# Performance work log

Hardware: AMD Instinct MI355X
Metric: run time of the kernel (lower is better)

The kernel has to match this reference:

```python
import jax, jax.numpy as jnp
import numpy as np

B, T, E = 4, 2048, 2048
H, KV = 16, 4
G = H // KV           # GQA group size
D = E // H            # head_dim = 128


def setup_inputs() -> dict:
    key = jax.random.key(0)
    kx, kq, kk, kv, ko = jax.random.split(key, 5)
    s = 1.0 / np.sqrt(E).astype(np.float32)
    x  = jax.random.normal(kx, (B, T, E), jnp.float32)
    Wq = jax.random.normal(kq, (E, H * D), jnp.float32) * s
    Wk = jax.random.normal(kk, (E, KV * D), jnp.float32) * s
    Wv = jax.random.normal(kv, (E, KV * D), jnp.float32) * s
    Wo = jax.random.normal(ko, (H * D, E), jnp.float32) * s
    return {"x": x, "Wq": Wq, "Wk": Wk, "Wv": Wv, "Wo": Wo}


def reference(x, Wq, Wk, Wv, Wo):
    # causal=True (default in the torch module)
    b, t, _ = x.shape
    scale = 1.0 / np.sqrt(D).astype(np.float32)
    # q heads ordered so that reshape (H,)->(KV,G) matches torch repeat_interleave
    q = (x @ Wq).reshape(b, t, KV, G, D)   # (B,T,KV,G,D)
    k = (x @ Wk).reshape(b, t, KV, D)      # (B,T,KV,D)
    v = (x @ Wv).reshape(b, t, KV, D)
    # scores per (kv-head h, group member g): (B,KV,G,T,T)
    scores = jnp.einsum('bqhgd,bkhd->bhgqk', q, k) * scale
    causal_mask = jnp.tril(jnp.ones((t, t), dtype=bool))  # True = keep
    scores = jnp.where(causal_mask, scores, -jnp.inf)
    w = jax.nn.softmax(scores, axis=-1)
    y = jnp.einsum('bhgqk,bkhd->bqhgd', w, v)  # (B,T,KV,G,D)
    y = y.reshape(b, t, H * D)
    return y @ Wo
```

## Files before the change

kernel.cpp:

```cpp
#include <hip/hip_runtime.h>

typedef unsigned short u16;
typedef __attribute__((ext_vector_type(8))) __bf16 bf16x8;
typedef __attribute__((ext_vector_type(4))) float f32x4;

#define BB 4
#define TT 2048
#define EE 2048
#define HH 16
#define KVH 4
#define DD 128

static __device__ __forceinline__ u16 f2bf(float f) {
  unsigned int u = __float_as_uint(f);
  u += 0x7fffu + ((u >> 16) & 1u);
  return (u16)(u >> 16);
}

static __device__ __forceinline__ void gl_lds16(const u16* g, u16* l) {
  __builtin_amdgcn_global_load_lds((__attribute__((address_space(1))) void*)g,
                                   (__attribute__((address_space(3))) void*)l,
                                   16, 0, 0);
}

__global__ __launch_bounds__(256) void cvt_f32_bf16(const float* __restrict__ in,
                                                    u16* __restrict__ out, int n4) {
  int i = blockIdx.x * 256 + threadIdx.x;
  if (i >= n4) return;
  float4 v = ((const float4*)in)[i];
  union { uint2 u2; u16 s[4]; } o;
  o.s[0] = f2bf(v.x); o.s[1] = f2bf(v.y); o.s[2] = f2bf(v.z); o.s[3] = f2bf(v.w);
  ((uint2*)out)[i] = o.u2;
}

__global__ __launch_bounds__(256) void transpose_w(const float* __restrict__ W,
                                                   u16* __restrict__ Wt, int R, int C) {
  __shared__ float tile[32][33];
  int tx = threadIdx.x & 31, ty = threadIdx.x >> 5;
  int r0 = blockIdx.y * 32, c0 = blockIdx.x * 32;
  #pragma unroll
  for (int i = ty; i < 32; i += 8)
    tile[i][tx] = W[(size_t)(r0 + i) * C + (c0 + tx)];
  __syncthreads();
  #pragma unroll
  for (int i = ty; i < 32; i += 8)
    Wt[(size_t)(c0 + i) * R + (r0 + tx)] = f2bf(tile[tx][i]);
}

__global__ __launch_bounds__(256) void transpose_v(const u16* __restrict__ KVb,
                                                   u16* __restrict__ VTg) {
  __shared__ u16 tile[32][36];
  const int tid = threadIdx.x;
  const int t0 = blockIdx.x * 32, d0 = blockIdx.y * 32;
  const int z = blockIdx.z;
  const int vb = z * 128;
  const size_t srcbase = (size_t)(z >> 2) * TT * 1024 + 512 + (z & 3) * 128;
  {
    int i = tid >> 3, c4 = (tid & 7) * 4;
    union { uint2 u; u16 s[4]; } r;
    r.u = *(const uint2*)(KVb + srcbase + (size_t)(t0 + i) * 1024 + d0 + c4);
    tile[i][c4] = r.s[0]; tile[i][c4 + 1] = r.s[1];
    tile[i][c4 + 2] = r.s[2]; tile[i][c4 + 3] = r.s[3];
  }
  __syncthreads();
  {
    int j = tid >> 3, cc = (tid & 7) * 4;
    union { uint2 u; u16 s[4]; } w;
    w.s[0] = tile[cc][j]; w.s[1] = tile[cc + 1][j];
    w.s[2] = tile[cc + 2][j]; w.s[3] = tile[cc + 3][j];
    *(uint2*)(VTg + (size_t)(vb + d0 + j) * TT + t0 + cc) = w.u;
  }
}

template <int MODE>
__global__ __launch_bounds__(512) void gemm256(const u16* __restrict__ A,
                                               const u16* __restrict__ Bt0,
                                               const u16* __restrict__ Bt1,
                                               void* __restrict__ C0,
                                               void* __restrict__ C1,
                                               int M, int N0, int N1, int K, int nbx) {
  __shared__ __align__(16) u16 sh[2][4][8192];
  const int tid = threadIdx.x;
  const int lane = tid & 63, wave = tid >> 6;
  const int quad = lane >> 4, n16 = lane & 15;
  const int mi = wave >> 2, ni = wave & 3;

  const int nwg = gridDim.x;
  int wg = blockIdx.x;
  wg = (wg & 7) * (nwg >> 3) + (wg >> 3);
  const int bx = wg % nbx, by = wg / nbx;
  const size_t rowbase = (size_t)by * 256;
  const int colbase = bx * 256;

  const u16* Bt = Bt0;
  int bcol = colbase;
  if (MODE == 1 && colbase >= N0) { Bt = Bt1; bcol = colbase - N0; }

  const int c0 = tid, c1 = tid + 512;
  const int r0s = c0 >> 3, ci0 = (c0 & 7) ^ (r0s & 7);
  const int r1s = c1 >> 3, ci1 = (c1 & 7) ^ (r1s & 7);
  const u16* Ag0 = A + (rowbase + r0s) * (size_t)K + ci0 * 8;
  const u16* Ag1 = A + (rowbase + r1s) * (size_t)K + ci1 * 8;
  const u16* Bg0 = Bt + ((size_t)bcol + r0s) * K + ci0 * 8;
  const u16* Bg1 = Bt + ((size_t)bcol + r1s) * K + ci1 * 8;
  const size_t h128K = (size_t)128 * K;

#define STAGE(ob, h, kb) do {                                              \
    if ((h) < 2) {                                                         \
      gl_lds16(Ag0 + (size_t)(h) * h128K + (kb), &sh[ob][h][c0 * 8]);      \
      gl_lds16(Ag1 + (size_t)(h) * h128K + (kb), &sh[ob][h][c1 * 8]);      \
    } else {                                                               \
      gl_lds16(Bg0 + (size_t)((h) - 2) * h128K + (kb), &sh[ob][h][c0 * 8]);\
      gl_lds16(Bg1 + (size_t)((h) - 2) * h128K + (kb), &sh[ob][h][c1 * 8]);\
    } } while (0)

#define LDA_HALF(mh) do {                                                  \
    _Pragma("unroll") for (int m = 0; m < 4; ++m)                          \
      _Pragma("unroll") for (int kk = 0; kk < 2; ++kk) {                   \
        int row_ = ((mh) * 4 + m) * 16 + n16;                              \
        int c_ = row_ * 8 + ((kk * 4 + quad) ^ (n16 & 7));                 \
        af[m][kk] = *(const bf16x8*)&sh[buf][mi][c_ * 8];                  \
      } } while (0)

#define LDB_HALF(nh, BF) do {                                              \
    _Pragma("unroll") for (int n = 0; n < 2; ++n)                          \
      _Pragma("unroll") for (int kk = 0; kk < 2; ++kk) {                   \
        int row_ = (ni & 1) * 64 + ((nh) * 2 + n) * 16 + n16;              \
        int c_ = row_ * 8 + ((kk * 4 + quad) ^ (n16 & 7));                 \
        BF[n][kk] = *(const bf16x8*)&sh[buf][2 + (ni >> 1)][c_ * 8];       \
      } } while (0)

#define DO_QUAD(mh, nh, BF) do {                                           \
    __builtin_amdgcn_s_setprio(1);                                         \
    _Pragma("unroll") for (int m = 0; m < 4; ++m)                          \
      _Pragma("unroll") for (int n = 0; n < 2; ++n)                        \
        _Pragma("unroll") for (int kk = 0; kk < 2; ++kk)                   \
          acc[(mh) * 4 + m][(nh) * 2 + n] =                                \
              __builtin_amdgcn_mfma_f32_16x16x32_bf16(                     \
                  af[m][kk], BF[n][kk], acc[(mh) * 4 + m][(nh) * 2 + n],   \
                  0, 0, 0);                                                \
    __builtin_amdgcn_s_setprio(0);                                         \
  } while (0)

#define FENCE() asm volatile("" ::: "memory")

  f32x4 acc[8][4];
  #pragma unroll
  for (int i = 0; i < 8; ++i)
    #pragma unroll
    for (int j = 0; j < 4; ++j) acc[i][j] = (f32x4){0.f, 0.f, 0.f, 0.f};

  bf16x8 af[4][2], bf0[2][2], bf1[2][2];
  const int nt = K / 64;

  STAGE(0, 0, 0); STAGE(0, 1, 0); STAGE(0, 2, 0); STAGE(0, 3, 0);

  #pragma unroll 2
  for (int t = 0; t < nt; ++t) {
    const int buf = t & 1, ob = buf ^ 1;
    const int kbn = (t + 1) * 64;
    const bool pre = (t + 1 < nt);

    if (pre) {
      STAGE(ob, 0, kbn);
      asm volatile("s_waitcnt vmcnt(2)" ::: "memory");
    } else {
      asm volatile("s_waitcnt vmcnt(0)" ::: "memory");
    }
    __builtin_amdgcn_s_barrier(); FENCE();
    LDA_HALF(0); LDB_HALF(0, bf0);
    DO_QUAD(0, 0, bf0);
    __builtin_amdgcn_s_barrier(); FENCE();

    LDB_HALF(1, bf1);
    if (pre) STAGE(ob, 1, kbn);
    __builtin_amdgcn_s_barrier(); FENCE();
    DO_QUAD(0, 1, bf1);
    __builtin_amdgcn_s_barrier(); FENCE();

    LDA_HALF(1);
    if (pre) STAGE(ob, 2, kbn);
    __builtin_amdgcn_s_barrier(); FENCE();
    DO_QUAD(1, 1, bf1);
    __builtin_amdgcn_s_barrier(); FENCE();

    if (pre) STAGE(ob, 3, kbn);
    __builtin_amdgcn_s_barrier(); FENCE();
    DO_QUAD(1, 0, bf0);
    __builtin_amdgcn_s_barrier(); FENCE();
  }

#undef STAGE
#undef LDA_HALF
#undef LDB_HALF
#undef DO_QUAD
#undef FENCE

  const size_t crow0 = rowbase + (size_t)mi * 128;
  #pragma unroll
  for (int mt = 0; mt < 8; ++mt) {
    #pragma unroll
    for (int r = 0; r < 4; ++r) {
      size_t row = crow0 + mt * 16 + quad * 4 + r;
      #pragma unroll
      for (int nt_ = 0; nt_ < 4; ++nt_) {
        int col = colbase + ni * 64 + nt_ * 16 + n16;
        float v = acc[mt][nt_][r];
        if (MODE == 0) {
          ((float*)C0)[row * (size_t)N0 + col] = v;
        } else {
          if (col < N0) ((u16*)C0)[row * (size_t)N0 + col] = f2bf(v);
          else          ((u16*)C1)[row * (size_t)N1 + (col - N0)] = f2bf(v);
        }
      }
    }
  }
}

__global__ __launch_bounds__(256) void attn_kernel(const u16* __restrict__ Qm,
                                                   const u16* __restrict__ KVm,
                                                   const u16* __restrict__ VTg,
                                                   u16* __restrict__ Ym) {
  __shared__ u16 Ks[32 * 128];
  __shared__ u16 Vt[128 * 32];
  __shared__ u16 Pb[4 * 32 * 40];

  const int tid = threadIdx.x;
  const int lane = tid & 63, wave = tid >> 6;
  const int quad = lane >> 4, n16 = lane & 15;
  const int b = blockIdx.y >> 4, h = blockIdx.y & 15;
  const int kvh = h >> 2;
  const int kvbase = b * TT;
  const u16* VTg_ = VTg + (size_t)((b * 4 + kvh) * 128) * TT;

  const int krow = tid >> 4, kslot = tid & 15;
  const int kg = (kslot ^ krow) * 8;
  u16* Ksd0 = &Ks[krow * 128 + kslot * 8];
  u16* Ksd1 = &Ks[(krow + 16) * 128 + kslot * 8];
  const int vrow = tid >> 2, vs = tid & 3;
  const int vq8 = (vs ^ ((tid >> 3) & 3)) * 8;
  u16* Vtd0 = &Vt[vrow * 32 + vs * 8];
  u16* Vtd1 = &Vt[(vrow + 64) * 32 + vs * 8];

  constexpr float SCL = 0.08838834764831843f * 1.4426950408889634f;

  for (int pass = 0; pass < 2; ++pass) {
    const int qt = pass ? 15 - (int)blockIdx.x : (int)blockIdx.x;
    const int q0 = qt * 128;
    const size_t qrowbase = (size_t)(b * TT + q0);
    const int wq0 = wave * 32;

    bf16x8 aq[2][4];
    #pragma unroll
    for (int mt = 0; mt < 2; ++mt) {
      const u16* qp = Qm + (qrowbase + wq0 + mt * 16 + n16) * (HH * DD) + h * DD + quad * 8;
      #pragma unroll
      for (int dt = 0; dt < 4; ++dt)
        aq[mt][dt] = *(const bf16x8*)(qp + dt * 32);
    }

    float lrow[2][4];
    f32x4 oacc[2][8];
    #pragma unroll
    for (int mt = 0; mt < 2; ++mt) {
      #pragma unroll
      for (int r = 0; r < 4; ++r) lrow[mt][r] = 0.f;
      #pragma unroll
      for (int i = 0; i < 8; ++i) oacc[mt][i] = (f32x4){0.f, 0.f, 0.f, 0.f};
    }

    const int kend = q0 + 128;
    for (int kb = 0; kb < kend; kb += 32) {
      __syncthreads();
      gl_lds16(KVm + (size_t)(kvbase + kb + krow) * 1024 + kvh * DD + kg, Ksd0);
      gl_lds16(KVm + (size_t)(kvbase + kb + krow + 16) * 1024 + kvh * DD + kg, Ksd1);
      gl_lds16(VTg_ + (size_t)vrow * TT + kb + vq8, Vtd0);
      gl_lds16(VTg_ + (size_t)(vrow + 64) * TT + kb + vq8, Vtd1);
      __syncthreads();

      f32x4 sf[2][2];
      #pragma unroll
      for (int half = 0; half < 2; ++half) {
        bf16x8 bk[4];
        #pragma unroll
        for (int dt = 0; dt < 4; ++dt) {
          int slot = (dt * 4 + quad) ^ n16;
          bk[dt] = *(const bf16x8*)&Ks[(half * 16 + n16) * 128 + slot * 8];
        }
        #pragma unroll
        for (int mt = 0; mt < 2; ++mt) {
          f32x4 s = (f32x4){0.f, 0.f, 0.f, 0.f};
          #pragma unroll
          for (int dt = 0; dt < 4; ++dt)
            s = __builtin_amdgcn_mfma_f32_16x16x32_bf16(aq[mt][dt], bk[dt], s, 0, 0, 0);
          sf[mt][half] = s;
        }
      }

      u16* pw = &Pb[wave * (32 * 40)];
      #pragma unroll
      for (int mt = 0; mt < 2; ++mt)
        #pragma unroll
        for (int half = 0; half < 2; ++half) {
          int key = kb + half * 16 + n16;
          #pragma unroll
          for (int r = 0; r < 4; ++r) {
            int qpos = q0 + wq0 + mt * 16 + quad * 4 + r;
            float pv = (key <= qpos) ? exp2f(sf[mt][half][r] * SCL) : 0.f;
            lrow[mt][r] += pv;
            pw[(mt * 16 + quad * 4 + r) * 40 + half * 16 + n16] = f2bf(pv);
          }
        }
      __builtin_amdgcn_s_waitcnt(0);
      bf16x8 ap[2];
      ap[0] = *(const bf16x8*)&pw[n16 * 40 + quad * 8];
      ap[1] = *(const bf16x8*)&pw[(16 + n16) * 40 + quad * 8];

      #pragma unroll
      for (int dt = 0; dt < 8; ++dt) {
        bf16x8 bv = *(const bf16x8*)&Vt[(dt * 16 + n16) * 32 +
                                        ((quad ^ ((n16 >> 1) & 3)) * 8)];
        oacc[0][dt] = __builtin_amdgcn_mfma_f32_16x16x32_bf16(ap[0], bv, oacc[0][dt], 0, 0, 0);
        oacc[1][dt] = __builtin_amdgcn_mfma_f32_16x16x32_bf16(ap[1], bv, oacc[1][dt], 0, 0, 0);
      }
    }

    float rinv[2][4];
    #pragma unroll
    for (int mt = 0; mt < 2; ++mt)
      #pragma unroll
      for (int r = 0; r < 4; ++r) {
        float v = lrow[mt][r];
        v += __shfl_xor(v, 1, 64);
        v += __shfl_xor(v, 2, 64);
        v += __shfl_xor(v, 4, 64);
        v += __shfl_xor(v, 8, 64);
        rinv[mt][r] = 1.0f / v;
      }
    #pragma unroll
    for (int mt = 0; mt < 2; ++mt)
      #pragma unroll
      for (int dt = 0; dt < 8; ++dt)
        #pragma unroll
        for (int r = 0; r < 4; ++r) {
          size_t row = qrowbase + wq0 + mt * 16 + quad * 4 + r;
          Ym[row * (HH * DD) + h * DD + dt * 16 + n16] = f2bf(oacc[mt][dt][r] * rinv[mt][r]);
        }
  }
}

extern "C" void kernel_launch(void* const* d_in, const int* in_sizes, int n_in,
                              void* d_out, int out_size, void* d_ws, size_t ws_size,
                              hipStream_t stream) {
  const float* x  = (const float*)d_in[0];
  const float* Wq = (const float*)d_in[1];
  const float* Wk = (const float*)d_in[2];
  const float* Wv = (const float*)d_in[3];
  const float* Wo = (const float*)d_in[4];
  float* out = (float*)d_out;

  u16* ws   = (u16*)d_ws;
  u16* xb   = ws;
  u16* Wbuf = xb + (size_t)8192 * 2048;
  u16* Yb   = xb;

  u16* ob   = (u16*)d_out;
  u16* Qb   = ob;
  u16* KVb  = ob + (size_t)8192 * 2048;
  u16* VTg  = ob + (size_t)8192 * 2048 + (size_t)8192 * 1024;
  u16* WkvT = VTg + (size_t)16 * 128 * 2048;

  cvt_f32_bf16<<<16384, 256, 0, stream>>>(x, xb, (4 * 2048 * 2048) / 4);

  transpose_w<<<dim3(64, 64), 256, 0, stream>>>(Wq, Wbuf, 2048, 2048);
  transpose_w<<<dim3(16, 64), 256, 0, stream>>>(Wk, WkvT, 2048, 512);
  transpose_w<<<dim3(16, 64), 256, 0, stream>>>(Wv, WkvT + (size_t)512 * 2048, 2048, 512);

  gemm256<1><<<384, 512, 0, stream>>>(xb, Wbuf, WkvT, (void*)Qb, (void*)KVb,
                                      8192, 2048, 1024, 2048, 12);

  transpose_v<<<dim3(64, 4, 16), 256, 0, stream>>>(KVb, VTg);

  attn_kernel<<<dim3(8, 64), 256, 0, stream>>>(Qb, KVb, VTg, Yb);

  transpose_w<<<dim3(64, 64), 256, 0, stream>>>(Wo, Wbuf, 2048, 2048);
  gemm256<0><<<256, 512, 0, stream>>>(Yb, Wbuf, nullptr, (void*)out, nullptr,
                                      8192, 2048, 0, 2048, 8);
}
```

Before: 475.6 us.

## Add 256x128-tile GEMM variant for the fused QKV projection

Adds a new GEMM kernel with a 256x128 output tile (8 waves, each computing 64x64) and uses it for the QKV projection, doubling the grid from 384 to 768 workgroups. The aim is to fill the many compute units more evenly and cut wave-quantization tail effects, since 384 large tiles map poorly onto the CU count. In exchange, each tile reuses its B data less, so global and LDS traffic per flop rise, and there are more barriers per k-step relative to the MFMA work.

Measured after the change: 470.7 us. No clear change (-1.0%).

```diff
diff --git a/kernel.cpp b/kernel.cpp
--- a/kernel.cpp
+++ b/kernel.cpp
@@ -199,6 +199,150 @@
   const size_t crow0 = rowbase + (size_t)mi * 128;
   #pragma unroll
   for (int mt = 0; mt < 8; ++mt) {
+    #pragma unroll
+    for (int r = 0; r < 4; ++r) {
+      size_t row = crow0 + mt * 16 + quad * 4 + r;
+      #pragma unroll
+      for (int nt_ = 0; nt_ < 4; ++nt_) {
+        int col = colbase + ni * 64 + nt_ * 16 + n16;
+        float v = acc[mt][nt_][r];
+        if (MODE == 0) {
+          ((float*)C0)[row * (size_t)N0 + col] = v;
+        } else {
+          if (col < N0) ((u16*)C0)[row * (size_t)N0 + col] = f2bf(v);
+          else          ((u16*)C1)[row * (size_t)N1 + (col - N0)] = f2bf(v);
+        }
+      }
+    }
+  }
+}
+
+template <int MODE>
+__global__ __launch_bounds__(512) void gemm_n128(const u16* __restrict__ A,
+                                                 const u16* __restrict__ Bt0,
+                                                 const u16* __restrict__ Bt1,
+                                                 void* __restrict__ C0,
+                                                 void* __restrict__ C1,
+                                                 int M, int N0, int N1, int K, int nbx) {
+  __shared__ __align__(16) u16 sh[2][3][8192];
+  const int tid = threadIdx.x;
+  const int lane = tid & 63, wave = tid >> 6;
+  const int quad = lane >> 4, n16 = lane & 15;
+  const int mi = wave >> 1, ni = wave & 1;
+
+  const int nwg = gridDim.x;
+  int wg = blockIdx.x;
+  wg = (wg & 7) * (nwg >> 3) + (wg >> 3);
+  const int bx = wg % nbx, by = wg / nbx;
+  const size_t rowbase = (size_t)by * 256;
+  const int colbase = bx * 128;
+
+  const u16* Bt = Bt0;
+  int bcol = colbase;
+  if (MODE == 1 && colbase >= N0) { Bt = Bt1; bcol = colbase - N0; }
+
+  const int c0 = tid, c1 = tid + 512;
+  const int r0s = c0 >> 3, ci0 = (c0 & 7) ^ (r0s & 7);
+  const int r1s = c1 >> 3, ci1 = (c1 & 7) ^ (r1s & 7);
+  const u16* Ag0 = A + (rowbase + r0s) * (size_t)K + ci0 * 8;
+  const u16* Ag1 = A + (rowbase + r1s) * (size_t)K + ci1 * 8;
+  const u16* Bg0 = Bt + ((size_t)bcol + r0s) * K + ci0 * 8;
+  const u16* Bg1 = Bt + ((size_t)bcol + r1s) * K + ci1 * 8;
+  const size_t h128K = (size_t)128 * K;
+
+#define STAGEN(ob, h, kb) do {                                             \
+    if ((h) < 2) {                                                         \
+      gl_lds16(Ag0 + (size_t)(h) * h128K + (kb), &sh[ob][h][c0 * 8]);      \
+      gl_lds16(Ag1 + (size_t)(h) * h128K + (kb), &sh[ob][h][c1 * 8]);      \
+    } else {                                                               \
+      gl_lds16(Bg0 + (kb), &sh[ob][2][c0 * 8]);                            \
+      gl_lds16(Bg1 + (kb), &sh[ob][2][c1 * 8]);                            \
+    } } while (0)
+
+#define LDAN(mh) do {                                                      \
+    _Pragma("unroll") for (int m = 0; m < 2; ++m)                          \
+      _Pragma("unroll") for (int kk = 0; kk < 2; ++kk) {                   \
+        int row_ = (mi & 1) * 64 + ((mh) * 2 + m) * 16 + n16;              \
+        int c_ = row_ * 8 + ((kk * 4 + quad) ^ (n16 & 7));                 \
+        af[m][kk] = *(const bf16x8*)&sh[buf][mi >> 1][c_ * 8];             \
+      } } while (0)
+
+#define LDBN(nh, BF) do {                                                  \
+    _Pragma("unroll") for (int n = 0; n < 2; ++n)                          \
+      _Pragma("unroll") for (int kk = 0; kk < 2; ++kk) {                   \
+        int row_ = ni * 64 + ((nh) * 2 + n) * 16 + n16;                    \
+        int c_ = row_ * 8 + ((kk * 4 + quad) ^ (n16 & 7));                 \
+        BF[n][kk] = *(const bf16x8*)&sh[buf][2][c_ * 8];                   \
+      } } while (0)
+
+#define QUADN(mh, nh, BF) do {                                             \
+    __builtin_amdgcn_s_setprio(1);                                         \
+    _Pragma("unroll") for (int m = 0; m < 2; ++m)                          \
+      _Pragma("unroll") for (int n = 0; n < 2; ++n)                        \
+        _Pragma("unroll") for (int kk = 0; kk < 2; ++kk)                   \
+          acc[(mh) * 2 + m][(nh) * 2 + n] =                                \
+              __builtin_amdgcn_mfma_f32_16x16x32_bf16(                     \
+                  af[m][kk], BF[n][kk], acc[(mh) * 2 + m][(nh) * 2 + n],   \
+                  0, 0, 0);                                                \
+    __builtin_amdgcn_s_setprio(0);                                         \
+  } while (0)
+
+#define FENCE() asm volatile("" ::: "memory")
+
+  f32x4 acc[4][4];
+  #pragma unroll
+  for (int i = 0; i < 4; ++i)
+    #pragma unroll
+    for (int j = 0; j < 4; ++j) acc[i][j] = (f32x4){0.f, 0.f, 0.f, 0.f};
+
+  bf16x8 af[2][2], bf0[2][2], bf1[2][2];
+  const int nt = K / 64;
+
+  STAGEN(0, 0, 0); STAGEN(0, 1, 0); STAGEN(0, 2, 0);
+
+  #pragma unroll 2
+  for (int t = 0; t < nt; ++t) {
+    const int buf = t & 1, ob = buf ^ 1;
+    const int kbn = (t + 1) * 64;
+    const bool pre = (t + 1 < nt);
+
+    if (pre) {
+      STAGEN(ob, 0, kbn);
+      asm volatile("s_waitcnt vmcnt(2)" ::: "memory");
+    } else {
+      asm volatile("s_waitcnt vmcnt(0)" ::: "memory");
+    }
+    __builtin_amdgcn_s_barrier(); FENCE();
+    LDAN(0); LDBN(0, bf0);
+    QUADN(0, 0, bf0);
+    __builtin_amdgcn_s_barrier(); FENCE();
+
+    LDBN(1, bf1);
+    if (pre) STAGEN(ob, 1, kbn);
+    __builtin_amdgcn_s_barrier(); FENCE();
+    QUADN(0, 1, bf1);
+    __builtin_amdgcn_s_barrier(); FENCE();
+
+    LDAN(1);
+    if (pre) STAGEN(ob, 2, kbn);
+    __builtin_amdgcn_s_barrier(); FENCE();
+    QUADN(1, 1, bf1);
+    __builtin_amdgcn_s_barrier(); FENCE();
+
+    __builtin_amdgcn_s_barrier(); FENCE();
+    QUADN(1, 0, bf0);
+    __builtin_amdgcn_s_barrier(); FENCE();
+  }
+
+#undef STAGEN
+#undef LDAN
+#undef LDBN
+#undef QUADN
+#undef FENCE
+
+  const size_t crow0 = rowbase + (size_t)mi * 64;
+  #pragma unroll
+  for (int mt = 0; mt < 4; ++mt) {
     #pragma unroll
     for (int r = 0; r < 4; ++r) {
       size_t row = crow0 + mt * 16 + quad * 4 + r;
@@ -376,8 +520,8 @@
   transpose_w<<<dim3(16, 64), 256, 0, stream>>>(Wk, WkvT, 2048, 512);
   transpose_w<<<dim3(16, 64), 256, 0, stream>>>(Wv, WkvT + (size_t)512 * 2048, 2048, 512);
 
-  gemm256<1><<<384, 512, 0, stream>>>(xb, Wbuf, WkvT, (void*)Qb, (void*)KVb,
-                                      8192, 2048, 1024, 2048, 12);
+  gemm_n128<1><<<768, 512, 0, stream>>>(xb, Wbuf, WkvT, (void*)Qb, (void*)KVb,
+                                        8192, 2048, 1024, 2048, 24);
 
   transpose_v<<<dim3(64, 4, 16), 256, 0, stream>>>(KVb, VTg);
 
```
